# Kernel optimization log

Hardware: AMD Instinct MI355X
Metric: run time of the kernel (lower is better)

Reference implementation:

```python
import jax, jax.numpy as jnp
import numpy as np

N_VISIBLE = 4096
N_HIDDEN = 4096
BATCH = 8192


def setup_inputs() -> dict:
    key = jax.random.key(0)
    k_x, k_w = jax.random.split(key)
    input_data = jax.random.uniform(k_x, (BATCH, N_VISIBLE), dtype=jnp.float32)
    # xavier_uniform with sigmoid gain (=1.0): limit = sqrt(6/(fan_in+fan_out))
    limit = float(np.sqrt(6.0 / (N_VISIBLE + N_HIDDEN)))
    W = jax.random.uniform(k_w, (N_VISIBLE, N_HIDDEN), dtype=jnp.float32,
                           minval=-limit, maxval=limit)
    hidden_bias = jnp.zeros((N_HIDDEN,), dtype=jnp.float32)
    return {"input_data": input_data, "W": W, "hidden_bias": hidden_bias}


def reference(input_data, W, hidden_bias):
    # RBM.sample_hidden_2 (forward): sigmoid(x @ W + b), batched over samples.
    # (The torch code loops per sample with host syncs; same math, vectorized.)
    hid_prob = jax.nn.sigmoid(jnp.matmul(input_data, W) + hidden_bias)
    return hid_prob
```

## Files before the change

kernel.cpp:

```cpp
#include <hip/hip_runtime.h>
#include <cstdint>

#define MDIM 8192
#define NDIM 4096
#define KDIM 4096

typedef __bf16 bf16x8 __attribute__((ext_vector_type(8)));
typedef float f32x4 __attribute__((ext_vector_type(4)));

__device__ __forceinline__ void gload_lds16(const void* g, void* l) {
    __builtin_amdgcn_global_load_lds(
        (const __attribute__((address_space(1))) uint32_t*)g,
        (__attribute__((address_space(3))) uint32_t*)l, 16, 0, 0);
}

__device__ __forceinline__ unsigned short bf16_bits(float f) {
    __bf16 b = (__bf16)f;
    return __builtin_bit_cast(unsigned short, b);
}

__device__ __forceinline__ int detect_f32(const void* X) {
    int ok = 1;
    if (threadIdx.x < 128) {
        unsigned short h = ((const unsigned short*)X)[threadIdx.x];
        ok = (h <= 0x3F80);
    }
    return __syncthreads_and(ok) ? 0 : 1;
}

__global__ __launch_bounds__(256) void prep(const void* __restrict__ X,
                                            const void* __restrict__ W,
                                            __bf16* __restrict__ Xb,
                                            __bf16* __restrict__ WT) {
    const int f32 = detect_f32(X);
    const int t = threadIdx.x;
    if (blockIdx.x < 8192) {
        if (!f32) return;
        const float* Xf = (const float*)X;
        const long base = ((long)blockIdx.x * 256 + t) * 16;
#pragma unroll
        for (int c = 0; c < 2; ++c) {
            float4 v0 = *(const float4*)(Xf + base + c * 8);
            float4 v1 = *(const float4*)(Xf + base + c * 8 + 4);
            unsigned short r[8] = {bf16_bits(v0.x), bf16_bits(v0.y),
                                   bf16_bits(v0.z), bf16_bits(v0.w),
                                   bf16_bits(v1.x), bf16_bits(v1.y),
                                   bf16_bits(v1.z), bf16_bits(v1.w)};
            *(uint4*)(Xb + base + c * 8) = *(const uint4*)r;
        }
        return;
    }
    __shared__ unsigned short tile[64 * 65];
    const int bid = blockIdx.x - 8192;
    const int n0 = (bid & 63) * 64;
    const int k0 = (bid >> 6) * 64;
    if (f32) {
        const float* Wf = (const float*)W;
#pragma unroll
        for (int p = 0; p < 4; ++p) {
            const int ch = p * 256 + t;
            const int kr = ch >> 4;
            const int nc = ch & 15;
            float4 v = *(const float4*)(Wf + (long)(k0 + kr) * NDIM + n0 + nc * 4);
            tile[(nc * 4 + 0) * 65 + kr] = bf16_bits(v.x);
            tile[(nc * 4 + 1) * 65 + kr] = bf16_bits(v.y);
            tile[(nc * 4 + 2) * 65 + kr] = bf16_bits(v.z);
            tile[(nc * 4 + 3) * 65 + kr] = bf16_bits(v.w);
        }
    } else {
        const __bf16* Wb = (const __bf16*)W;
#pragma unroll
        for (int p = 0; p < 2; ++p) {
            const int ch = p * 256 + t;
            const int kr = ch >> 3;
            const int nc = ch & 7;
            uint4 v = *(const uint4*)(Wb + (long)(k0 + kr) * NDIM + n0 + nc * 8);
            const unsigned short* e = (const unsigned short*)&v;
#pragma unroll
            for (int i = 0; i < 8; ++i) tile[(nc * 8 + i) * 65 + kr] = e[i];
        }
    }
    __syncthreads();
#pragma unroll
    for (int p = 0; p < 2; ++p) {
        const int ch = p * 256 + t;
        const int nr = ch >> 3;
        const int kc = ch & 7;
        unsigned short r[8];
#pragma unroll
        for (int i = 0; i < 8; ++i) r[i] = tile[nr * 65 + kc * 8 + i];
        *(uint4*)(WT + (long)(n0 + nr) * KDIM + k0 + kc * 8) = *(uint4*)r;
    }
}

__global__ __launch_bounds__(256) void transpose_w(const void* __restrict__ X,
                                                   const void* __restrict__ W,
                                                   __bf16* __restrict__ WT) {
    __shared__ unsigned short tile[64 * 65];
    const int f32 = detect_f32(X);
    const int t = threadIdx.x;
    const int k0 = blockIdx.y * 64;
    const int n0 = blockIdx.x * 64;
    if (f32) {
        const float* Wf = (const float*)W;
#pragma unroll
        for (int p = 0; p < 4; ++p) {
            const int ch = p * 256 + t;
            const int kr = ch >> 4;
            const int nc = ch & 15;
            float4 v = *(const float4*)(Wf + (long)(k0 + kr) * NDIM + n0 + nc * 4);
            tile[(nc * 4 + 0) * 65 + kr] = bf16_bits(v.x);
            tile[(nc * 4 + 1) * 65 + kr] = bf16_bits(v.y);
            tile[(nc * 4 + 2) * 65 + kr] = bf16_bits(v.z);
            tile[(nc * 4 + 3) * 65 + kr] = bf16_bits(v.w);
        }
    } else {
        const __bf16* Wb = (const __bf16*)W;
#pragma unroll
        for (int p = 0; p < 2; ++p) {
            const int ch = p * 256 + t;
            const int kr = ch >> 3;
            const int nc = ch & 7;
            uint4 v = *(const uint4*)(Wb + (long)(k0 + kr) * NDIM + n0 + nc * 8);
            const unsigned short* e = (const unsigned short*)&v;
#pragma unroll
            for (int i = 0; i < 8; ++i) tile[(nc * 8 + i) * 65 + kr] = e[i];
        }
    }
    __syncthreads();
#pragma unroll
    for (int p = 0; p < 2; ++p) {
        const int ch = p * 256 + t;
        const int nr = ch >> 3;
        const int kc = ch & 7;
        unsigned short r[8];
#pragma unroll
        for (int i = 0; i < 8; ++i) r[i] = tile[nr * 65 + kc * 8 + i];
        *(uint4*)(WT + (long)(n0 + nr) * KDIM + k0 + kc * 8) = *(uint4*)r;
    }
}

template <int MODE>
__global__ __launch_bounds__(256) void gemm_bias_sigmoid(
    const void* __restrict__ X, const __bf16* __restrict__ Xb,
    const void* __restrict__ Wp, const __bf16* __restrict__ WT,
    const void* __restrict__ bias, void* __restrict__ out) {
    __shared__ __bf16 sA[128 * 64];
    __shared__ __bf16 sB[128 * 64];
    const int f32 = detect_f32(X);
    const int t = threadIdx.x;
    const int lane = t & 63;
    const int wid = t >> 6;
    const int m0 = blockIdx.y * 128;
    const int n0 = blockIdx.x * 128;
    const int wm = (wid & 1) * 64;
    const int wn = (wid >> 1) * 64;
    const int lrow = lane & 15;
    const int quad = lane >> 4;

    f32x4 acc[4][4] = {};

    if constexpr (MODE == 0) {
        const __bf16* Abf = f32 ? Xb : (const __bf16*)X;
        const int r8 = lane >> 3;
        const int c8 = lane & 7;
        const int cs = (c8 ^ r8) * 8;
        const __bf16* gA = Abf + (long)(m0 + wid * 32 + r8) * KDIM + cs;
        const __bf16* gB = WT + (long)(n0 + wid * 32 + r8) * KDIM + cs;
        __bf16* lA = sA + wid * 32 * 64;
        __bf16* lB = sB + wid * 32 * 64;
        const int l7 = lrow & 7;
        const __bf16* pa0 = sA + (wm + lrow) * 64;
        const __bf16* pb0 = sB + (wn + lrow) * 64;
        const int sw[8] = {(0 ^ l7) * 8, (1 ^ l7) * 8, (2 ^ l7) * 8,
                           (3 ^ l7) * 8, (4 ^ l7) * 8, (5 ^ l7) * 8,
                           (6 ^ l7) * 8, (7 ^ l7) * 8};

        for (int kt = 0; kt < KDIM / 64; ++kt) {
            const int kb = kt * 64;
#pragma unroll
            for (int i = 0; i < 4; ++i) {
                gload_lds16(gA + kb + (long)(i * 8) * KDIM, lA + i * 512);
                gload_lds16(gB + kb + (long)(i * 8) * KDIM, lB + i * 512);
            }
            __syncthreads();
#pragma unroll
            for (int h = 0; h < 2; ++h) {
                bf16x8 aF[4], bF[4];
                const int so = sw[h * 4 + quad];
#pragma unroll
                for (int i = 0; i < 4; ++i)
                    aF[i] = *(const bf16x8*)(pa0 + i * 1024 + so);
#pragma unroll
                for (int j = 0; j < 4; ++j)
                    bF[j] = *(const bf16x8*)(pb0 + j * 1024 + so);
#pragma unroll
                for (int i = 0; i < 4; ++i)
#pragma unroll
                    for (int j = 0; j < 4; ++j)
                        acc[i][j] = __builtin_amdgcn_mfma_f32_16x16x32_bf16(
                            aF[i], bF[j], acc[i][j], 0, 0, 0);
            }
            __syncthreads();
        }
    } else {
        const int srow = t >> 2;
        const int schk = t & 3;
        __bf16* ldsA = sA + wid * 512;
        __bf16* ldsB = sB + wid * 512;
        const int arow = t >> 1;
        const int acol = (t & 1) * 16;
        const int fp = t & 15;
        const int fc = t >> 4;
        uint32_t* sB32 = (uint32_t*)sB;

        auto compute = [&]() {
            bf16x8 aF[4], bF[4];
            const __bf16* pa = sA + (wm + lrow) * 32 + quad * 8;
            const __bf16* pb = sB + (wn + lrow) * 32 + quad * 8;
#pragma unroll
            for (int i = 0; i < 4; ++i) aF[i] = *(const bf16x8*)(pa + i * 512);
#pragma unroll
            for (int j = 0; j < 4; ++j) bF[j] = *(const bf16x8*)(pb + j * 512);
#pragma unroll
            for (int i = 0; i < 4; ++i)
#pragma unroll
                for (int j = 0; j < 4; ++j)
                    acc[i][j] = __builtin_amdgcn_mfma_f32_16x16x32_bf16(
                        aF[i], bF[j], acc[i][j], 0, 0, 0);
        };

        if (MODE == 1 && !f32) {
            const __bf16* gA = (const __bf16*)X + (long)(m0 + srow) * KDIM + schk * 8;
            const __bf16* gB = WT + (long)(n0 + srow) * KDIM + schk * 8;
            for (int kt = 0; kt < KDIM / 32; ++kt) {
                const __bf16* a0 = gA + kt * 32;
                gload_lds16(a0, ldsA);
                gload_lds16(a0 + (long)64 * KDIM, ldsA + 2048);
                const __bf16* b0 = gB + kt * 32;
                gload_lds16(b0, ldsB);
                gload_lds16(b0 + (long)64 * KDIM, ldsB + 2048);
                __syncthreads();
                compute();
                __syncthreads();
            }
        } else if (MODE == 1) {
            const float* Xf = (const float*)X;
            const __bf16* gB = WT + (long)(n0 + srow) * KDIM + schk * 8;
            for (int kt = 0; kt < KDIM / 32; ++kt) {
                const __bf16* b0 = gB + kt * 32;
                gload_lds16(b0, ldsB);
                gload_lds16(b0 + (long)64 * KDIM, ldsB + 2048);
                const float* ap = Xf + (long)(m0 + arow) * KDIM + kt * 32 + acol;
                float4 v0 = *(const float4*)(ap);
                float4 v1 = *(const float4*)(ap + 4);
                float4 v2 = *(const float4*)(ap + 8);
                float4 v3 = *(const float4*)(ap + 12);
                unsigned short r[16] = {
                    bf16_bits(v0.x), bf16_bits(v0.y), bf16_bits(v0.z), bf16_bits(v0.w),
                    bf16_bits(v1.x), bf16_bits(v1.y), bf16_bits(v1.z), bf16_bits(v1.w),
                    bf16_bits(v2.x), bf16_bits(v2.y), bf16_bits(v2.z), bf16_bits(v2.w),
                    bf16_bits(v3.x), bf16_bits(v3.y), bf16_bits(v3.z), bf16_bits(v3.w)};
                *(uint4*)(sA + arow * 32 + acol) = *(const uint4*)(r);
                *(uint4*)(sA + arow * 32 + acol + 8) = *(const uint4*)(r + 8);
                __syncthreads();
                compute();
                __syncthreads();
            }
        } else if (MODE == 2 && !f32) {
            const __bf16* gA = (const __bf16*)X + (long)(m0 + srow) * KDIM + schk * 8;
            const __bf16* Wb = (const __bf16*)Wp;
            for (int kt = 0; kt < KDIM / 32; ++kt) {
                const __bf16* a0 = gA + kt * 32;
                gload_lds16(a0, ldsA);
                gload_lds16(a0 + (long)64 * KDIM, ldsA + 2048);
                const __bf16* w0 = Wb + (long)(kt * 32 + 2 * fp) * NDIM + n0 + fc * 8;
                uint4 g0 = *(const uint4*)(w0);
                uint4 g1 = *(const uint4*)(w0 + NDIM);
                const unsigned short* e0 = (const unsigned short*)&g0;
                const unsigned short* e1 = (const unsigned short*)&g1;
#pragma unroll
                for (int i = 0; i < 8; ++i)
                    sB32[(fc * 8 + i) * 16 + fp] =
                        (uint32_t)e0[i] | ((uint32_t)e1[i] << 16);
                __syncthreads();
                compute();
                __syncthreads();
            }
        } else if (MODE == 2) {
            const float* Xf = (const float*)X;
            const float* Wf = (const float*)Wp;
            for (int kt = 0; kt < KDIM / 32; ++kt) {
                const float* ap = Xf + (long)(m0 + arow) * KDIM + kt * 32 + acol;
                float4 v0 = *(const float4*)(ap);
                float4 v1 = *(const float4*)(ap + 4);
                float4 v2 = *(const float4*)(ap + 8);
                float4 v3 = *(const float4*)(ap + 12);
                unsigned short r[16] = {
                    bf16_bits(v0.x), bf16_bits(v0.y), bf16_bits(v0.z), bf16_bits(v0.w),
                    bf16_bits(v1.x), bf16_bits(v1.y), bf16_bits(v1.z), bf16_bits(v1.w),
                    bf16_bits(v2.x), bf16_bits(v2.y), bf16_bits(v2.z), bf16_bits(v2.w),
                    bf16_bits(v3.x), bf16_bits(v3.y), bf16_bits(v3.z), bf16_bits(v3.w)};
                *(uint4*)(sA + arow * 32 + acol) = *(const uint4*)(r);
                *(uint4*)(sA + arow * 32 + acol + 8) = *(const uint4*)(r + 8);
                const float* w0 = Wf + (long)(kt * 32 + 2 * fp) * NDIM + n0 + fc * 8;
                float4 u0 = *(const float4*)(w0);
                float4 u1 = *(const float4*)(w0 + 4);
                float4 u2 = *(const float4*)(w0 + NDIM);
                float4 u3 = *(const float4*)(w0 + NDIM + 4);
                float k0v[8] = {u0.x, u0.y, u0.z, u0.w, u1.x, u1.y, u1.z, u1.w};
                float k1v[8] = {u2.x, u2.y, u2.z, u2.w, u3.x, u3.y, u3.z, u3.w};
#pragma unroll
                for (int i = 0; i < 8; ++i)
                    sB32[(fc * 8 + i) * 16 + fp] =
                        (uint32_t)bf16_bits(k0v[i]) |
                        ((uint32_t)bf16_bits(k1v[i]) << 16);
                __syncthreads();
                compute();
                __syncthreads();
            }
        }
    }

    const int crow = m0 + wm + quad * 4;
    if (f32) {
        float* of = (float*)out;
        const float* bf = (const float*)bias;
#pragma unroll
        for (int j = 0; j < 4; ++j) {
            const int col = n0 + wn + j * 16 + lrow;
            const float bv = bf[col];
#pragma unroll
            for (int i = 0; i < 4; ++i) {
                const long rbase = (long)(crow + i * 16) * NDIM + col;
#pragma unroll
                for (int r = 0; r < 4; ++r) {
                    const float x = acc[i][j][r] + bv;
                    of[rbase + (long)r * NDIM] = 1.0f / (1.0f + __expf(-x));
                }
            }
        }
    } else {
        __bf16* ob = (__bf16*)out;
        const __bf16* bb = (const __bf16*)bias;
#pragma unroll
        for (int j = 0; j < 4; ++j) {
            const int col = n0 + wn + j * 16 + lrow;
            const float bv = (float)bb[col];
#pragma unroll
            for (int i = 0; i < 4; ++i) {
                const long rbase = (long)(crow + i * 16) * NDIM + col;
#pragma unroll
                for (int r = 0; r < 4; ++r) {
                    const float x = acc[i][j][r] + bv;
                    ob[rbase + (long)r * NDIM] = (__bf16)(1.0f / (1.0f + __expf(-x)));
                }
            }
        }
    }
}

extern "C" void kernel_launch(void* const* d_in, const int* in_sizes, int n_in,
                              void* d_out, int out_size, void* d_ws,
                              size_t ws_size, hipStream_t stream) {
    const void* X = d_in[0];
    const void* W = d_in[1];
    const void* bias = d_in[2];

    const size_t wt_bytes = (size_t)KDIM * NDIM * sizeof(__bf16);
    const size_t xb_bytes = (size_t)MDIM * KDIM * sizeof(__bf16);
    dim3 gg(NDIM / 128, MDIM / 128);

    if (ws_size >= wt_bytes + xb_bytes) {
        __bf16* WT = (__bf16*)d_ws;
        __bf16* Xb = (__bf16*)((char*)d_ws + wt_bytes);
        prep<<<8192 + 4096, 256, 0, stream>>>(X, W, Xb, WT);
        gemm_bias_sigmoid<0><<<gg, 256, 0, stream>>>(X, Xb, W, WT, bias, d_out);
    } else if (ws_size >= wt_bytes) {
        __bf16* WT = (__bf16*)d_ws;
        transpose_w<<<dim3(NDIM / 64, KDIM / 64), 256, 0, stream>>>(X, W, WT);
        gemm_bias_sigmoid<1><<<gg, 256, 0, stream>>>(X, nullptr, W, WT, bias, d_out);
    } else {
        gemm_bias_sigmoid<2><<<gg, 256, 0, stream>>>(X, nullptr, W, nullptr, bias, d_out);
    }
}
```

Before: 590.9 us.

## Add 256x256 double-buffered 8-wave GEMM with interleaved loads and block swizzle

Replaces the 128x128 single-buffered MODE 0 GEMM with a new 512-thread kernel that computes 256x256 tiles and double-buffers LDS. Global-to-LDS loads for future k-steps are interleaved between MFMA phases, using explicit barriers, waitcnt and setprio to overlap memory with compute. A grid swizzle is added to improve L2 reuse. In exchange, register and LDS pressure is much higher (128 KB of LDS, 32 accumulators per lane), and hand-placed waitcnt and barriers risk races if the vmcnt accounting is wrong.

```diff
diff --git a/kernel.cpp b/kernel.cpp
--- a/kernel.cpp
+++ b/kernel.cpp
@@ -4,9 +4,12 @@
 #define MDIM 8192
 #define NDIM 4096
 #define KDIM 4096
+#define NT (KDIM / 64)
 
 typedef __bf16 bf16x8 __attribute__((ext_vector_type(8)));
 typedef float f32x4 __attribute__((ext_vector_type(4)));
+
+#define MFMA16 __builtin_amdgcn_mfma_f32_16x16x32_bf16
 
 __device__ __forceinline__ void gload_lds16(const void* g, void* l) {
     __builtin_amdgcn_global_load_lds(
@@ -137,6 +140,192 @@
 #pragma unroll
         for (int i = 0; i < 8; ++i) r[i] = tile[nr * 65 + kc * 8 + i];
         *(uint4*)(WT + (long)(n0 + nr) * KDIM + k0 + kc * 8) = *(uint4*)r;
+    }
+}
+
+#define P_OPEN()                                        \
+    do {                                                \
+        __builtin_amdgcn_sched_barrier(0);              \
+        __builtin_amdgcn_s_barrier();                   \
+        asm volatile("s_waitcnt lgkmcnt(0)" ::: "memory"); \
+        __builtin_amdgcn_sched_barrier(0);              \
+    } while (0)
+#define P_CLOSE()                          \
+    do {                                   \
+        __builtin_amdgcn_sched_barrier(0); \
+        __builtin_amdgcn_s_barrier();      \
+    } while (0)
+
+__global__ __launch_bounds__(512, 2) void gemm256(
+    const void* __restrict__ X, const __bf16* __restrict__ Xb,
+    const __bf16* __restrict__ WT, const void* __restrict__ bias,
+    void* __restrict__ out) {
+    __shared__ __bf16 sA[2][256][64];
+    __shared__ __bf16 sB[2][256][64];
+    const int f32 = detect_f32(X);
+    const __bf16* __restrict__ Abf = f32 ? Xb : (const __bf16*)X;
+    const int t = threadIdx.x;
+    const int lane = t & 63;
+    const int wid = t >> 6;
+    const int wm = wid >> 2;
+    const int wn = wid & 3;
+    const int lrow = lane & 15;
+    const int quad = lane >> 4;
+    const int l7 = lrow & 7;
+
+    const int flat = blockIdx.x;
+    const int swz = (flat & 7) * (512 / 8) + (flat >> 3);
+    const long m0 = (long)(swz >> 4) * 256;
+    const long n0 = (long)(swz & 15) * 256;
+
+    const int r8 = lane >> 3;
+    const int c8 = lane & 7;
+    const int cs = (c8 ^ r8) * 8;
+    const __bf16* gA = Abf + (m0 + wid * 8 + r8) * KDIM + cs;
+    const __bf16* gB = WT + (n0 + wid * 8 + r8) * KDIM + cs;
+    __bf16* lA = &sA[0][wid * 8][0];
+    __bf16* lB = &sB[0][wid * 8][0];
+
+    auto stage_a = [&](int tt2) {
+        const long off = (long)(tt2 & 1) * 16384;
+        const long ko = (long)(tt2 & (NT - 1)) * 64;
+        gload_lds16(gA + ko, lA + off);
+        gload_lds16(gA + (long)64 * KDIM + ko, lA + off + 4096);
+        gload_lds16(gA + (long)128 * KDIM + ko, lA + off + 8192);
+        gload_lds16(gA + (long)192 * KDIM + ko, lA + off + 12288);
+    };
+    auto stage_b = [&](int tt2, int h) {
+        const long off = (long)(tt2 & 1) * 16384 + (long)h * 8192;
+        const long ko = (long)(tt2 & (NT - 1)) * 64;
+        gload_lds16(gB + (long)(h * 128) * KDIM + ko, lB + off);
+        gload_lds16(gB + (long)(h * 128 + 64) * KDIM + ko, lB + off + 4096);
+    };
+
+    const int soff0 = (quad ^ l7) * 8;
+    const int soff1 = ((4 + quad) ^ l7) * 8;
+    const __bf16* pa = &sA[0][wm * 128 + lrow][0];
+    const __bf16* pb = &sB[0][wn * 64 + lrow][0];
+
+    f32x4 acc[8][4] = {};
+
+    stage_a(0);
+    stage_b(0, 0);
+    stage_b(0, 1);
+    stage_b(1, 0);
+    stage_a(1);
+    __builtin_amdgcn_sched_barrier(0);
+    asm volatile("s_waitcnt vmcnt(6)" ::: "memory");
+    __builtin_amdgcn_sched_barrier(0);
+    __builtin_amdgcn_s_barrier();
+
+#pragma unroll 1
+    for (int tt = 0; tt < NT; ++tt) {
+        const int db = tt & 1;
+        const __bf16* paT = pa + db * 16384;
+        const __bf16* pbT = pb + db * 16384;
+        bf16x8 aF[4][2], bF[4][2];
+#pragma unroll
+        for (int j = 0; j < 4; ++j) {
+            bF[j][0] = *(const bf16x8*)(pbT + j * 1024 + soff0);
+            bF[j][1] = *(const bf16x8*)(pbT + j * 1024 + soff1);
+        }
+#pragma unroll
+        for (int i = 0; i < 4; ++i) {
+            aF[i][0] = *(const bf16x8*)(paT + i * 1024 + soff0);
+            aF[i][1] = *(const bf16x8*)(paT + i * 1024 + soff1);
+        }
+        stage_b(tt + 1, 1);
+        P_OPEN();
+        __builtin_amdgcn_s_setprio(1);
+#pragma unroll
+        for (int i = 0; i < 4; ++i)
+#pragma unroll
+            for (int j = 0; j < 2; ++j) {
+                acc[i][j] = MFMA16(aF[i][0], bF[j][0], acc[i][j], 0, 0, 0);
+                acc[i][j] = MFMA16(aF[i][1], bF[j][1], acc[i][j], 0, 0, 0);
+            }
+        __builtin_amdgcn_s_setprio(0);
+        P_CLOSE();
+        stage_b(tt + 2, 0);
+        P_OPEN();
+        __builtin_amdgcn_s_setprio(1);
+#pragma unroll
+        for (int i = 0; i < 4; ++i)
+#pragma unroll
+            for (int j = 2; j < 4; ++j) {
+                acc[i][j] = MFMA16(aF[i][0], bF[j][0], acc[i][j], 0, 0, 0);
+                acc[i][j] = MFMA16(aF[i][1], bF[j][1], acc[i][j], 0, 0, 0);
+            }
+        __builtin_amdgcn_s_setprio(0);
+        P_CLOSE();
+#pragma unroll
+        for (int i = 0; i < 4; ++i) {
+            aF[i][0] = *(const bf16x8*)(paT + 4096 + i * 1024 + soff0);
+            aF[i][1] = *(const bf16x8*)(paT + 4096 + i * 1024 + soff1);
+        }
+        P_OPEN();
+        __builtin_amdgcn_s_setprio(1);
+#pragma unroll
+        for (int i = 0; i < 4; ++i)
+#pragma unroll
+            for (int j = 2; j < 4; ++j) {
+                acc[i + 4][j] = MFMA16(aF[i][0], bF[j][0], acc[i + 4][j], 0, 0, 0);
+                acc[i + 4][j] = MFMA16(aF[i][1], bF[j][1], acc[i + 4][j], 0, 0, 0);
+            }
+        __builtin_amdgcn_s_setprio(0);
+        P_CLOSE();
+        stage_a(tt + 2);
+        P_OPEN();
+        __builtin_amdgcn_s_setprio(1);
+#pragma unroll
+        for (int i = 0; i < 4; ++i)
+#pragma unroll
+            for (int j = 0; j < 2; ++j) {
+                acc[i + 4][j] = MFMA16(aF[i][0], bF[j][0], acc[i + 4][j], 0, 0, 0);
+                acc[i + 4][j] = MFMA16(aF[i][1], bF[j][1], acc[i + 4][j], 0, 0, 0);
+            }
+        __builtin_amdgcn_s_setprio(0);
+        __builtin_amdgcn_sched_barrier(0);
+        asm volatile("s_waitcnt vmcnt(6)" ::: "memory");
+        __builtin_amdgcn_sched_barrier(0);
+        __builtin_amdgcn_s_barrier();
+    }
+
+    const int crow0 = (int)m0 + wm * 128 + quad * 4;
+    if (f32) {
+        float* of = (float*)out;
+        const float* bf = (const float*)bias;
+#pragma unroll
+        for (int j = 0; j < 4; ++j) {
+            const int col = (int)n0 + wn * 64 + j * 16 + lrow;
+            const float bv = bf[col];
+#pragma unroll
+            for (int i = 0; i < 8; ++i) {
+                const long rbase = (long)(crow0 + i * 16) * NDIM + col;
+#pragma unroll
+                for (int r = 0; r < 4; ++r) {
+                    const float x = acc[i][j][r] + bv;
+                    of[rbase + (long)r * NDIM] = 1.0f / (1.0f + __expf(-x));
+                }
+            }
+        }
+    } else {
+        __bf16* ob = (__bf16*)out;
+        const __bf16* bb = (const __bf16*)bias;
+#pragma unroll
+        for (int j = 0; j < 4; ++j) {
+            const int col = (int)n0 + wn * 64 + j * 16 + lrow;
+            const float bv = (float)bb[col];
+#pragma unroll
+            for (int i = 0; i < 8; ++i) {
+                const long rbase = (long)(crow0 + i * 16) * NDIM + col;
+#pragma unroll
+                for (int r = 0; r < 4; ++r) {
+                    const float x = acc[i][j][r] + bv;
+                    ob[rbase + (long)r * NDIM] = (__bf16)(1.0f / (1.0f + __expf(-x)));
+                }
+            }
+        }
     }
 }
 
@@ -160,50 +349,7 @@
 
     f32x4 acc[4][4] = {};
 
-    if constexpr (MODE == 0) {
-        const __bf16* Abf = f32 ? Xb : (const __bf16*)X;
-        const int r8 = lane >> 3;
-        const int c8 = lane & 7;
-        const int cs = (c8 ^ r8) * 8;
-        const __bf16* gA = Abf + (long)(m0 + wid * 32 + r8) * KDIM + cs;
-        const __bf16* gB = WT + (long)(n0 + wid * 32 + r8) * KDIM + cs;
-        __bf16* lA = sA + wid * 32 * 64;
-        __bf16* lB = sB + wid * 32 * 64;
-        const int l7 = lrow & 7;
-        const __bf16* pa0 = sA + (wm + lrow) * 64;
-        const __bf16* pb0 = sB + (wn + lrow) * 64;
-        const int sw[8] = {(0 ^ l7) * 8, (1 ^ l7) * 8, (2 ^ l7) * 8,
-                           (3 ^ l7) * 8, (4 ^ l7) * 8, (5 ^ l7) * 8,
-                           (6 ^ l7) * 8, (7 ^ l7) * 8};
-
-        for (int kt = 0; kt < KDIM / 64; ++kt) {
-            const int kb = kt * 64;
-#pragma unroll
-            for (int i = 0; i < 4; ++i) {
-                gload_lds16(gA + kb + (long)(i * 8) * KDIM, lA + i * 512);
-                gload_lds16(gB + kb + (long)(i * 8) * KDIM, lB + i * 512);
-            }
-            __syncthreads();
-#pragma unroll
-            for (int h = 0; h < 2; ++h) {
-                bf16x8 aF[4], bF[4];
-                const int so = sw[h * 4 + quad];
-#pragma unroll
-                for (int i = 0; i < 4; ++i)
-                    aF[i] = *(const bf16x8*)(pa0 + i * 1024 + so);
-#pragma unroll
-                for (int j = 0; j < 4; ++j)
-                    bF[j] = *(const bf16x8*)(pb0 + j * 1024 + so);
-#pragma unroll
-                for (int i = 0; i < 4; ++i)
-#pragma unroll
-                    for (int j = 0; j < 4; ++j)
-                        acc[i][j] = __builtin_amdgcn_mfma_f32_16x16x32_bf16(
-                            aF[i], bF[j], acc[i][j], 0, 0, 0);
-            }
-            __syncthreads();
-        }
-    } else {
+    {
         const int srow = t >> 2;
         const int schk = t & 3;
         __bf16* ldsA = sA + wid * 512;
@@ -215,19 +361,18 @@
         uint32_t* sB32 = (uint32_t*)sB;
 
         auto compute = [&]() {
-            bf16x8 aF[4], bF[4];
+            bf16x8 aF[4], bFr[4];
             const __bf16* pa = sA + (wm + lrow) * 32 + quad * 8;
             const __bf16* pb = sB + (wn + lrow) * 32 + quad * 8;
 #pragma unroll
             for (int i = 0; i < 4; ++i) aF[i] = *(const bf16x8*)(pa + i * 512);
 #pragma unroll
-            for (int j = 0; j < 4; ++j) bF[j] = *(const bf16x8*)(pb + j * 512);
+            for (int j = 0; j < 4; ++j) bFr[j] = *(const bf16x8*)(pb + j * 512);
 #pragma unroll
             for (int i = 0; i < 4; ++i)
 #pragma unroll
                 for (int j = 0; j < 4; ++j)
-                    acc[i][j] = __builtin_amdgcn_mfma_f32_16x16x32_bf16(
-                        aF[i], bF[j], acc[i][j], 0, 0, 0);
+                    acc[i][j] = MFMA16(aF[i], bFr[j], acc[i][j], 0, 0, 0);
         };
 
         if (MODE == 1 && !f32) {
@@ -369,18 +514,20 @@
 
     const size_t wt_bytes = (size_t)KDIM * NDIM * sizeof(__bf16);
     const size_t xb_bytes = (size_t)MDIM * KDIM * sizeof(__bf16);
-    dim3 gg(NDIM / 128, MDIM / 128);
 
     if (ws_size >= wt_bytes + xb_bytes) {
         __bf16* WT = (__bf16*)d_ws;
         __bf16* Xb = (__bf16*)((char*)d_ws + wt_bytes);
         prep<<<8192 + 4096, 256, 0, stream>>>(X, W, Xb, WT);
-        gemm_bias_sigmoid<0><<<gg, 256, 0, stream>>>(X, Xb, W, WT, bias, d_out);
+        gemm256<<<dim3((MDIM / 256) * (NDIM / 256)), 512, 0, stream>>>(
+            X, Xb, WT, bias, d_out);
     } else if (ws_size >= wt_bytes) {
         __bf16* WT = (__bf16*)d_ws;
         transpose_w<<<dim3(NDIM / 64, KDIM / 64), 256, 0, stream>>>(X, W, WT);
+        dim3 gg(NDIM / 128, MDIM / 128);
         gemm_bias_sigmoid<1><<<gg, 256, 0, stream>>>(X, nullptr, W, WT, bias, d_out);
     } else {
+        dim3 gg(NDIM / 128, MDIM / 128);
         gemm_bias_sigmoid<2><<<gg, 256, 0, stream>>>(X, nullptr, W, nullptr, bias, d_out);
     }
 }
```

New measurement: 559.3 us. 5.3% less time.
